# Kernel optimization log

Hardware: AMD Instinct MI355X
Metric: run time of the kernel (lower is better)

## Reference

```python
import jax, jax.numpy as jnp
import numpy as np


def _rope_tables(T, half):
    # theta_i = 10000^(-i/half), standard RoPE frequencies for head_size=2*half
    thetas = 10000.0 ** (-jnp.arange(half, dtype=jnp.float32) / half)  # (half,)
    ang = jnp.arange(T, dtype=jnp.float32)[:, None] * thetas[None, :]  # (T, half)
    return jnp.sin(ang), jnp.cos(ang)


def _apply_rope(x, sin, cos):
    # x: (B, H, T, hs); sin/cos: (T, hs//2). Interleaved pair rotation.
    xe = x[..., 0::2]
    xo = x[..., 1::2]
    s = sin[None, None, :, :]
    c = cos[None, None, :, :]
    re = xe * c - xo * s
    ro = xe * s + xo * c
    return jnp.stack([re, ro], axis=-1).reshape(x.shape)


def setup_inputs() -> dict:
    key = jax.random.key(0)
    ks = jax.random.split(key, 5)
    B, T, C, H = 4, 2048, 1024, 16
    scale = 1.0 / np.sqrt(C)
    x = jax.random.normal(ks[0], (B, T, C), dtype=jnp.float32)
    Wqkv = jax.random.normal(ks[1], (C, 3 * C), dtype=jnp.float32) * scale
    bqkv = jax.random.normal(ks[2], (3 * C,), dtype=jnp.float32) * 0.01
    Wout = jax.random.normal(ks[3], (C, C), dtype=jnp.float32) * scale
    bout = jax.random.normal(ks[4], (C,), dtype=jnp.float32) * 0.01
    return {"x": x, "Wqkv": Wqkv, "bqkv": bqkv, "Wout": Wout, "bout": bout,
            "num_heads": H}


def reference(x, Wqkv, bqkv, Wout, bout, num_heads) -> jnp.ndarray:
    B, T, C = x.shape
    H = num_heads
    hs = C // H
    norm = 1.0 / np.sqrt(hs)

    qkv = x @ Wqkv + bqkv                       # (B, T, 3C)
    qkv = qkv.reshape(B, T, 3, H, hs)
    qkv = jnp.transpose(qkv, (0, 3, 2, 1, 4))   # (B, H, 3, T, hs) = transpose(1,3)
    q, k, v = qkv[:, :, 0], qkv[:, :, 1], qkv[:, :, 2]  # each (B, H, T, hs)

    sin, cos = _rope_tables(T, hs // 2)
    q = _apply_rope(q, sin, cos)
    k = _apply_rope(k, sin, cos)

    att = jnp.einsum('bhqd,bhkd->bhqk', q, k) * norm  # (B, H, T, T)
    causal = jnp.triu(jnp.ones((T, T), dtype=bool), k=1)
    att = jnp.where(causal[None, None], -jnp.inf, att)
    att_prob = jax.nn.softmax(att, axis=-1)

    out = jnp.einsum('bhqk,bhkd->bhqd', att_prob, v)  # (B, H, T, hs)
    out = jnp.transpose(out, (0, 2, 1, 3)).reshape(B, T, C)
    return out @ Wout + bout
```

## Files before the change

kernel.cpp:

```cpp
#include <hip/hip_runtime.h>
#include <math.h>

#define B_   4
#define T_   2048
#define C_   1024
#define H_   16
#define HS   64
#define HALF 32
#define QKV_N (3 * C_)
#define M_    (B_ * T_)

using bf16x8 = __attribute__((ext_vector_type(8))) short;
using f32x4  = __attribute__((ext_vector_type(4))) float;
using f32x16 = __attribute__((ext_vector_type(16))) float;
using u16x4  = __attribute__((ext_vector_type(4))) unsigned short;
using u32x2  = __attribute__((ext_vector_type(2))) unsigned int;

__device__ __forceinline__ unsigned short f2bf(float f) {
    unsigned u = __builtin_bit_cast(unsigned, f);
    u = (u + 0x7FFFu + ((u >> 16) & 1u)) >> 16;
    return (unsigned short)u;
}
__device__ __forceinline__ float bf2f(unsigned short b) {
    return __builtin_bit_cast(float, (unsigned)b << 16);
}
__device__ __forceinline__ unsigned cvtpk_bf16(float lo, float hi_) {
    unsigned r;
    asm("v_cvt_pk_bf16_f32 %0, %1, %2" : "=v"(r) : "v"(lo), "v"(hi_));
    return r;
}
__device__ __forceinline__ void gload16(const void* g, void* l) {
    __builtin_amdgcn_global_load_lds(
        (const __attribute__((address_space(1))) unsigned int*)g,
        (__attribute__((address_space(3))) unsigned int*)l, 16, 0, 0);
}
#define WAIT_VMCNT_8() asm volatile("s_waitcnt vmcnt(8)" ::: "memory")
#define WAIT_VMCNT_4() asm volatile("s_waitcnt vmcnt(4)" ::: "memory")
#define WAIT_VMCNT_0() asm volatile("s_waitcnt vmcnt(0)" ::: "memory")

#if __has_builtin(__builtin_amdgcn_exp2f)
#define EXP2(x) __builtin_amdgcn_exp2f(x)
#else
#define EXP2(x) exp2f(x)
#endif
#define FMAX3(a, b, c) fmaxf(fmaxf((a), (b)), (c))

#define QSCALE 0.18033688011112042f

__global__ __launch_bounds__(256) void prep2_kernel(
    const float* __restrict__ x, unsigned short* __restrict__ xb,
    float2* __restrict__ tab,
    const float* __restrict__ Wqkv, const float* __restrict__ Wout,
    unsigned short* __restrict__ Wqkvt, unsigned short* __restrict__ Woutt)
{
    __shared__ float tile[32][33];
    const int bid = blockIdx.x;
    if (bid < 4096) {
        const size_t i = ((size_t)bid * 256 + threadIdx.x) * 8;
        const float4 a = *reinterpret_cast<const float4*>(&x[i]);
        const float4 b = *reinterpret_cast<const float4*>(&x[i + 4]);
        bf16x8 v;
        v[0] = f2bf(a.x); v[1] = f2bf(a.y); v[2] = f2bf(a.z); v[3] = f2bf(a.w);
        v[4] = f2bf(b.x); v[5] = f2bf(b.y); v[6] = f2bf(b.z); v[7] = f2bf(b.w);
        *reinterpret_cast<bf16x8*>(&xb[i]) = v;
        return;
    }
    if (bid < 4352) {
        const int idx = (bid - 4096) * 256 + threadIdx.x;
        const int t = idx / HALF;
        const int i = idx % HALF;
        const float theta = powf(10000.0f, -(float)i / (float)HALF);
        const float ang = (float)t * theta;
        float sn, cs;
        sincosf(ang, &sn, &cs);
        tab[idx] = make_float2(sn, cs);
        return;
    }
    const float* W;
    unsigned short* Wt;
    int N, k0, n0;
    if (bid < 7424) {
        const int r0 = bid - 4352;
        W = Wqkv; Wt = Wqkvt; N = QKV_N;
        n0 = (r0 % 96) * 32; k0 = (r0 / 96) * 32;
    } else {
        const int r0 = bid - 7424;
        W = Wout; Wt = Woutt; N = C_;
        n0 = (r0 % 32) * 32; k0 = (r0 / 32) * 32;
    }
    const int K = C_;
    const int r = threadIdx.x / 32;
    const int c = threadIdx.x % 32;
    #pragma unroll
    for (int it = 0; it < 4; ++it)
        tile[r + it * 8][c] = W[(size_t)(k0 + r + it * 8) * N + n0 + c];
    __syncthreads();
    #pragma unroll
    for (int it = 0; it < 4; ++it)
        Wt[(size_t)(n0 + r + it * 8) * K + k0 + c] = f2bf(tile[c][r + it * 8]);
}

template <int N, int K, bool BF16OUT, bool ROPE, bool VSPLIT>
__global__ __launch_bounds__(256, 4) void gemm_mfma_kernel(
    const unsigned short* __restrict__ A, const unsigned short* __restrict__ Bt,
    const float* __restrict__ bias, const float2* __restrict__ tab,
    void* __restrict__ Cout, unsigned short* __restrict__ vt, int nbx, int nby)
{
    __shared__ unsigned short As[2][128 * 32];
    __shared__ unsigned short Bs[2][128 * 32];

    const int tid  = threadIdx.x;
    const int lane = tid & 63;
    const int wave = tid >> 6;
    const int wr   = wave >> 1;
    const int wc   = wave & 1;
    const int l15  = lane & 15;
    const int l4   = lane >> 4;

    const int bid  = blockIdx.x;
    const int xcd  = bid & 7;
    const int w    = bid >> 3;
    const int cpr  = nbx >> 1;
    const int rpr  = nby >> 2;
    const int by   = ((xcd >> 1) * rpr) + (w / cpr);
    const int bx   = ((xcd & 1) * cpr) + (w % cpr);
    const int row0 = by * 128;
    const int col0 = bx * 128;

    f32x4 acc[4][4] = {};

    const int ar  = tid >> 2;
    const int sl  = tid & 3;
    const int swz = (sl ^ ((ar >> 1) & 3)) * 8;
    const unsigned short* ap = &A[(size_t)(row0 + ar) * K + swz];
    const unsigned short* bp = &Bt[(size_t)(col0 + ar) * K + swz];

    auto stage = [&](int buf, int t) {
        const unsigned short* a0 = ap + t * 32;
        const unsigned short* b0 = bp + t * 32;
        gload16(a0,          &As[buf][tid * 8]);
        gload16(a0 + 64 * K, &As[buf][(tid + 256) * 8]);
        gload16(b0,          &Bs[buf][tid * 8]);
        gload16(b0 + 64 * K, &Bs[buf][(tid + 256) * 8]);
    };

    int aoff[4], boff[4];
    #pragma unroll
    for (int mi = 0; mi < 4; ++mi) {
        const int lr = wr * 64 + mi * 16 + l15;
        aoff[mi] = lr * 32 + ((l4 ^ ((lr >> 1) & 3)) * 8);
    }
    #pragma unroll
    for (int nj = 0; nj < 4; ++nj) {
        const int lr = wc * 64 + nj * 16 + l15;
        boff[nj] = lr * 32 + ((l4 ^ ((lr >> 1) & 3)) * 8);
    }

    constexpr int nt = K / 32;
    stage(0, 0);

    for (int t = 0; t < nt; ++t) {
        const int cur = t & 1;
        if (t + 1 < nt) {
            stage(cur ^ 1, t + 1);
            WAIT_VMCNT_4();
        } else {
            WAIT_VMCNT_0();
        }
        __builtin_amdgcn_s_barrier();
        __builtin_amdgcn_sched_barrier(0);

        bf16x8 a[4], b[4];
        #pragma unroll
        for (int mi = 0; mi < 4; ++mi)
            a[mi] = *reinterpret_cast<const bf16x8*>(&As[cur][aoff[mi]]);
        #pragma unroll
        for (int nj = 0; nj < 4; ++nj)
            b[nj] = *reinterpret_cast<const bf16x8*>(&Bs[cur][boff[nj]]);
        #pragma unroll
        for (int mi = 0; mi < 4; ++mi)
            #pragma unroll
            for (int nj = 0; nj < 4; ++nj)
                acc[mi][nj] = __builtin_amdgcn_mfma_f32_16x16x32_bf16(
                    a[mi], b[nj], acc[mi][nj], 0, 0, 0);

        __builtin_amdgcn_sched_barrier(0);
        __builtin_amdgcn_s_barrier();
    }

    float bv[4];
    #pragma unroll
    for (int nj = 0; nj < 4; ++nj)
        bv[nj] = bias[col0 + wc * 64 + nj * 16 + l15];

    if (VSPLIT && col0 >= 2 * C_) {
        #pragma unroll
        for (int mi = 0; mi < 4; ++mi) {
            const int rowb = row0 + wr * 64 + mi * 16 + l4 * 4;
            const int b  = rowb >> 11;
            const int t0 = rowb & (T_ - 1);
            #pragma unroll
            for (int nj = 0; nj < 4; ++nj) {
                const int cv = col0 - 2 * C_ + wc * 64 + nj * 16 + l15;
                u16x4 pack;
                #pragma unroll
                for (int r = 0; r < 4; ++r)
                    pack[r] = f2bf(acc[mi][nj][r] + bv[nj]);
                *reinterpret_cast<u16x4*>(
                    &vt[((size_t)(b * H_ * HS + cv)) * T_ + t0]) = pack;
            }
        }
        return;
    }

    const bool doRope = ROPE && (col0 < 2 * C_);
    const bool doScaleQ = ROPE && (col0 < C_);

    #pragma unroll
    for (int mi = 0; mi < 4; ++mi) {
        #pragma unroll
        for (int r = 0; r < 4; ++r) {
            const int row = row0 + wr * 64 + mi * 16 + l4 * 4 + r;
            const int t   = row & (T_ - 1);
            #pragma unroll
            for (int nj = 0; nj < 4; ++nj) {
                const int col = col0 + wc * 64 + nj * 16 + l15;
                float v = acc[mi][nj][r] + bv[nj];
                if (doRope) {
                    const float partner = __shfl_xor(v, 1);
                    const float2 sc = tab[t * HALF + ((col & 63) >> 1)];
                    v = v * sc.y + ((col & 1) ? partner : -partner) * sc.x;
                }
                if (doScaleQ) v *= QSCALE;
                if (BF16OUT)
                    ((unsigned short*)Cout)[(size_t)row * N + col] = f2bf(v);
                else
                    ((float*)Cout)[(size_t)row * N + col] = v;
            }
        }
    }
}

__global__ __launch_bounds__(256, 2) void attn_mfma5_kernel(
    const unsigned short* __restrict__ qkv,
    const unsigned short* __restrict__ vt,
    unsigned short* __restrict__ out)
{
    __shared__ unsigned short Ks[2][128 * 64];
    __shared__ unsigned short Vs[2][64 * 128];

    const int idx = blockIdx.x;
    const int bh  = idx & 63;
    const int qp  = idx >> 6;
    const int b   = bh >> 4;
    const int h   = bh & 15;
    const int qtA = qp;
    const int qtB = 15 - qp;

    const int tid  = threadIdx.x;
    const int lane = tid & 63;
    const int w    = tid >> 6;
    const int l31  = lane & 31;
    const int hi   = lane >> 5;

    const int qwA = qtA * 128 + w * 32;
    const int qgA = qwA + l31;
    const int qwB = qtB * 128 + w * 32;
    const int qgB = qwB + l31;

    bf16x8 aqA[4], aqB[4];
    {
        const unsigned short* qpA = &qkv[(size_t)(b * T_ + qgA) * QKV_N + h * HS + hi * 8];
        const unsigned short* qpB = &qkv[(size_t)(b * T_ + qgB) * QKV_N + h * HS + hi * 8];
        #pragma unroll
        for (int kc = 0; kc < 4; ++kc) {
            aqA[kc] = *reinterpret_cast<const bf16x8*>(qpA + kc * 16);
            aqB[kc] = *reinterpret_cast<const bf16x8*>(qpB + kc * 16);
        }
    }

    f32x16 accA0 = {}, accA1 = {}, accB0 = {}, accB1 = {};
    float mA = -INFINITY, lA = 0.f, mB = -INFINITY, lB = 0.f;

    auto stageKV = [&](int buf, int it) {
        #pragma unroll
        for (int n = 0; n < 4; ++n) {
            const int r  = n * 32 + (tid >> 3);
            const int sk = ((tid & 7) ^ (r & 7)) * 8;
            gload16(&qkv[(size_t)(b * T_ + it * 128 + r) * QKV_N + C_ + h * HS + sk],
                    &Ks[buf][(n * 256 + tid) * 8]);
        }
        #pragma unroll
        for (int n = 0; n < 4; ++n) {
            const int d  = n * 16 + (tid >> 4);
            const int sv = ((tid & 15) ^ (d & 7)) * 8;
            gload16(&vt[((size_t)(bh * HS + d)) * T_ + it * 128 + sv],
                    &Vs[buf][(n * 256 + tid) * 8]);
        }
    };

    auto process = [&](const unsigned short* Kb, const unsigned short* Vb,
                       const bf16x8* aq, f32x16& a0, f32x16& a1,
                       float& mval, float& lval, int qw, int qg, int kbase) {
        f32x16 s[4] = {};
        __builtin_amdgcn_s_setprio(1);
        #pragma unroll
        for (int kc = 0; kc < 4; ++kc) {
            const int bo = kc * 32 + hi * 16;
            #pragma unroll
            for (int g = 0; g < 4; ++g) {
                const int rj = g * 32 + l31;
                const bf16x8 ak = *reinterpret_cast<const bf16x8*>(
                    &Kb[rj * 64 + ((bo ^ ((rj & 7) << 4)) >> 1)]);
                s[g] = __builtin_amdgcn_mfma_f32_32x32x16_bf16(ak, aq[kc], s[g], 0, 0, 0);
            }
        }
        __builtin_amdgcn_s_setprio(0);

        if (kbase + 127 > qw) {
            #pragma unroll
            for (int g = 0; g < 4; ++g) {
                #pragma unroll
                for (int r = 0; r < 16; ++r) {
                    const int j0 = kbase + g * 32 + (r & 3) + 8 * (r >> 2) + 4 * hi;
                    if (j0 > qg) s[g][r] = -INFINITY;
                }
            }
        }

        float tg[4];
        #pragma unroll
        for (int g = 0; g < 4; ++g) {
            const float v0 = FMAX3(s[g][0],  s[g][1],  s[g][2]);
            const float v1 = FMAX3(s[g][3],  s[g][4],  s[g][5]);
            const float v2 = FMAX3(s[g][6],  s[g][7],  s[g][8]);
            const float v3 = FMAX3(s[g][9],  s[g][10], s[g][11]);
            const float v4 = FMAX3(s[g][12], s[g][13], s[g][14]);
            tg[g] = fmaxf(FMAX3(v0, v1, v2), FMAX3(v3, v4, s[g][15]));
        }
        float tm = fmaxf(fmaxf(tg[0], tg[1]), fmaxf(tg[2], tg[3]));
        tm = fmaxf(tm, __shfl_xor(tm, 32));

        const bool upd = (tm > mval + 8.f);
        if (__ballot(upd)) {
            const float nm = upd ? tm : mval;
            const float sf = EXP2(mval - nm);
            lval *= sf;
            #pragma unroll
            for (int r = 0; r < 16; ++r) { a0[r] *= sf; a1[r] *= sf; }
            mval = nm;
        }

        float rs0 = 0.f, rs1 = 0.f, rs2 = 0.f, rs3 = 0.f;
        #pragma unroll
        for (int r = 0; r < 16; ++r) {
            s[0][r] = EXP2(s[0][r] - mval); rs0 += s[0][r];
            s[1][r] = EXP2(s[1][r] - mval); rs1 += s[1][r];
            s[2][r] = EXP2(s[2][r] - mval); rs2 += s[2][r];
            s[3][r] = EXP2(s[3][r] - mval); rs3 += s[3][r];
        }
        float rs = (rs0 + rs1) + (rs2 + rs3);
        rs += __shfl_xor(rs, 32);
        lval += rs;

        #pragma unroll
        for (int g2 = 0; g2 < 2; ++g2) {
            #pragma unroll
            for (int jt = 0; jt < 2; ++jt) {
                const int g = g2 * 2 + jt;
                #pragma unroll
                for (int c = 0; c < 2; ++c) {
                    const int e = c * 8;
                    const unsigned pa = cvtpk_bf16(s[g][e + 0], s[g][e + 1]);
                    const unsigned pb = cvtpk_bf16(s[g][e + 2], s[g][e + 3]);
                    const unsigned pc = cvtpk_bf16(s[g][e + 4], s[g][e + 5]);
                    const unsigned pd = cvtpk_bf16(s[g][e + 6], s[g][e + 7]);
                    int4 bw;
#if __has_builtin(__builtin_amdgcn_permlane32_swap)
                    const u32x2 rx = __builtin_amdgcn_permlane32_swap(pa, pc, false, false);
                    const u32x2 ry = __builtin_amdgcn_permlane32_swap(pb, pd, false, false);
                    bw.x = (int)rx[0]; bw.y = (int)ry[0];
                    bw.z = (int)rx[1]; bw.w = (int)ry[1];
#else
                    const unsigned pas = (unsigned)__shfl_xor((int)pa, 32);
                    const unsigned pbs = (unsigned)__shfl_xor((int)pb, 32);
                    const unsigned pcs = (unsigned)__shfl_xor((int)pc, 32);
                    const unsigned pds = (unsigned)__shfl_xor((int)pd, 32);
                    bw.x = (int)(hi ? pcs : pa);
                    bw.y = (int)(hi ? pds : pb);
                    bw.z = (int)(hi ? pc  : pas);
                    bw.w = (int)(hi ? pd  : pbs);
#endif
                    const bf16x8 bfrag = __builtin_bit_cast(bf16x8, bw);

                    const int lslot = g2 * 8 + (jt * 2 + c) * 2 + hi;
                    const int d0 = l31;
                    const bf16x8 av0 = *reinterpret_cast<const bf16x8*>(
                        &Vb[d0 * 128 + (lslot ^ (d0 & 7)) * 8]);
                    const int d1 = 32 + l31;
                    const bf16x8 av1 = *reinterpret_cast<const bf16x8*>(
                        &Vb[d1 * 128 + (lslot ^ (d1 & 7)) * 8]);
                    __builtin_amdgcn_s_setprio(1);
                    a0 = __builtin_amdgcn_mfma_f32_32x32x16_bf16(av0, bfrag, a0, 0, 0, 0);
                    a1 = __builtin_amdgcn_mfma_f32_32x32x16_bf16(av1, bfrag, a1, 0, 0, 0);
                    __builtin_amdgcn_s_setprio(0);
                }
            }
        }
    };

    const int nIter = qtB + 1;
    stageKV(0, 0);
    for (int it = 0; it < nIter; ++it) {
        const int cur = it & 1;
        __builtin_amdgcn_sched_barrier(0);
        if (it + 1 < nIter) {
            stageKV(cur ^ 1, it + 1);
            WAIT_VMCNT_8();
        } else {
            WAIT_VMCNT_0();
        }
        __builtin_amdgcn_s_barrier();
        __builtin_amdgcn_sched_barrier(0);

        const unsigned short* Kb = &Ks[cur][0];
        const unsigned short* Vb = &Vs[cur][0];
        const int kbase = it * 128;
        if (kbase <= qwA + 31)
            process(Kb, Vb, aqA, accA0, accA1, mA, lA, qwA, qgA, kbase);
        if (kbase <= qwB + 31)
            process(Kb, Vb, aqB, accB0, accB1, mB, lB, qwB, qgB, kbase);
        __builtin_amdgcn_sched_barrier(0);
        __builtin_amdgcn_s_barrier();
    }

    {
        const float inv = 1.0f / lA;
        unsigned short* orow = &out[(size_t)(b * T_ + qgA) * C_ + h * HS];
        #pragma unroll
        for (int g = 0; g < 4; ++g) {
            uint2 wv;
            wv.x = cvtpk_bf16(accA0[4 * g + 0] * inv, accA0[4 * g + 1] * inv);
            wv.y = cvtpk_bf16(accA0[4 * g + 2] * inv, accA0[4 * g + 3] * inv);
            *reinterpret_cast<uint2*>(&orow[8 * g + 4 * hi]) = wv;
            uint2 wv1;
            wv1.x = cvtpk_bf16(accA1[4 * g + 0] * inv, accA1[4 * g + 1] * inv);
            wv1.y = cvtpk_bf16(accA1[4 * g + 2] * inv, accA1[4 * g + 3] * inv);
            *reinterpret_cast<uint2*>(&orow[32 + 8 * g + 4 * hi]) = wv1;
        }
    }
    {
        const float inv = 1.0f / lB;
        unsigned short* orow = &out[(size_t)(b * T_ + qgB) * C_ + h * HS];
        #pragma unroll
        for (int g = 0; g < 4; ++g) {
            uint2 wv;
            wv.x = cvtpk_bf16(accB0[4 * g + 0] * inv, accB0[4 * g + 1] * inv);
            wv.y = cvtpk_bf16(accB0[4 * g + 2] * inv, accB0[4 * g + 3] * inv);
            *reinterpret_cast<uint2*>(&orow[8 * g + 4 * hi]) = wv;
            uint2 wv1;
            wv1.x = cvtpk_bf16(accB1[4 * g + 0] * inv, accB1[4 * g + 1] * inv);
            wv1.y = cvtpk_bf16(accB1[4 * g + 2] * inv, accB1[4 * g + 3] * inv);
            *reinterpret_cast<uint2*>(&orow[32 + 8 * g + 4 * hi]) = wv1;
        }
    }
}

extern "C" void kernel_launch(void* const* d_in, const int* in_sizes, int n_in,
                              void* d_out, int out_size, void* d_ws, size_t ws_size,
                              hipStream_t stream)
{
    const float* x    = (const float*)d_in[0];
    const float* Wqkv = (const float*)d_in[1];
    const float* bqkv = (const float*)d_in[2];
    const float* Wout = (const float*)d_in[3];
    const float* bout = (const float*)d_in[4];
    float* out = (float*)d_out;

    char* ws = (char*)d_ws;
    unsigned short* qkvb  = (unsigned short*)ws;
    unsigned short* xb    = (unsigned short*)(ws + 50331648);
    unsigned short* attnb = (unsigned short*)(ws + 67108864);
    unsigned short* vt_g  = (unsigned short*)(ws + 83886080);
    unsigned short* Wqkvt = (unsigned short*)(ws + 100663296);
    unsigned short* Woutt = (unsigned short*)(ws + 106954752);
    float2* tab           = (float2*)(ws + 109051904);

    prep2_kernel<<<8448, 256, 0, stream>>>(x, xb, tab, Wqkv, Wout, Wqkvt, Woutt);

    gemm_mfma_kernel<QKV_N, C_, true, true, true>
        <<<(M_ / 128) * (QKV_N / 128), 256, 0, stream>>>(
        xb, Wqkvt, bqkv, tab, qkvb, vt_g, QKV_N / 128, M_ / 128);

    attn_mfma5_kernel<<<B_ * H_ * (T_ / 256), 256, 0, stream>>>(qkvb, vt_g, attnb);

    gemm_mfma_kernel<C_, C_, false, false, false>
        <<<(M_ / 128) * (C_ / 128), 256, 0, stream>>>(
        attnb, Woutt, bout, nullptr, out, nullptr, C_ / 128, M_ / 128);
}
```

Before: 167.2 us.

## Replace GEMMs with 256x256-tile, 8-wave, four-phase ping-pong MFMA kernel

Both projection GEMMs move from 128x128 tiles with 4 waves to 256x256 tiles with 8 waves and a BK of 64. The K loop is split into four phases, each issuing one quarter-tile global-to-LDS prefetch and then running one 128x64 quadrant of MFMAs, with s_setprio raising priority around the MFMA bursts. The aim is more operand reuse per LDS byte and better overlap of loads with compute. The cost is 128 KB of LDS per block, one block per CU, and far fewer blocks: the output projection launches only 128 blocks and the QKV projection 384, which risks underfilling the GPU or leaving a tail wave.

```diff
diff --git a/kernel.cpp b/kernel.cpp
--- a/kernel.cpp
+++ b/kernel.cpp
@@ -37,6 +37,7 @@
 #define WAIT_VMCNT_8() asm volatile("s_waitcnt vmcnt(8)" ::: "memory")
 #define WAIT_VMCNT_4() asm volatile("s_waitcnt vmcnt(4)" ::: "memory")
 #define WAIT_VMCNT_0() asm volatile("s_waitcnt vmcnt(0)" ::: "memory")
+#define WAIT_LGKM_0()  asm volatile("s_waitcnt lgkmcnt(0)" ::: "memory")
 
 #if __has_builtin(__builtin_amdgcn_exp2f)
 #define EXP2(x) __builtin_amdgcn_exp2f(x)
@@ -101,19 +102,21 @@
 }
 
 template <int N, int K, bool BF16OUT, bool ROPE, bool VSPLIT>
-__global__ __launch_bounds__(256, 4) void gemm_mfma_kernel(
+__global__ __launch_bounds__(512, 1) void gemm_8ph_kernel(
     const unsigned short* __restrict__ A, const unsigned short* __restrict__ Bt,
     const float* __restrict__ bias, const float2* __restrict__ tab,
     void* __restrict__ Cout, unsigned short* __restrict__ vt, int nbx, int nby)
 {
-    __shared__ unsigned short As[2][128 * 32];
-    __shared__ unsigned short Bs[2][128 * 32];
+    __shared__ unsigned short As0[2][128 * 64];
+    __shared__ unsigned short As1[2][128 * 64];
+    __shared__ unsigned short Bs0[2][128 * 64];
+    __shared__ unsigned short Bs1[2][128 * 64];
 
     const int tid  = threadIdx.x;
     const int lane = tid & 63;
     const int wave = tid >> 6;
-    const int wr   = wave >> 1;
-    const int wc   = wave & 1;
+    const int wr   = wave >> 2;
+    const int wc   = wave & 3;
     const int l15  = lane & 15;
     const int l4   = lane >> 4;
 
@@ -124,88 +127,176 @@
     const int rpr  = nby >> 2;
     const int by   = ((xcd >> 1) * rpr) + (w / cpr);
     const int bx   = ((xcd & 1) * cpr) + (w % cpr);
-    const int row0 = by * 128;
-    const int col0 = bx * 128;
-
-    f32x4 acc[4][4] = {};
-
-    const int ar  = tid >> 2;
-    const int sl  = tid & 3;
-    const int swz = (sl ^ ((ar >> 1) & 3)) * 8;
-    const unsigned short* ap = &A[(size_t)(row0 + ar) * K + swz];
-    const unsigned short* bp = &Bt[(size_t)(col0 + ar) * K + swz];
-
-    auto stage = [&](int buf, int t) {
-        const unsigned short* a0 = ap + t * 32;
-        const unsigned short* b0 = bp + t * 32;
-        gload16(a0,          &As[buf][tid * 8]);
-        gload16(a0 + 64 * K, &As[buf][(tid + 256) * 8]);
-        gload16(b0,          &Bs[buf][tid * 8]);
-        gload16(b0 + 64 * K, &Bs[buf][(tid + 256) * 8]);
+    const int row0 = by * 256;
+    const int col0 = bx * 256;
+
+    const int lr0 = tid >> 3,          sl0 = tid & 7;
+    const int lr1 = (tid + 512) >> 3,  sl1 = (tid + 512) & 7;
+    const int kc0 = (sl0 ^ (lr0 & 7)) * 8;
+    const int kc1 = (sl1 ^ (lr1 & 7)) * 8;
+    const int dA0 = tid * 8;
+    const int dA1 = (tid + 512) * 8;
+    const unsigned short* apS0 = &A[(size_t)(row0 + (lr0 >> 6) * 128 + (lr0 & 63)) * K + kc0];
+    const unsigned short* apS1 = &A[(size_t)(row0 + (lr1 >> 6) * 128 + (lr1 & 63)) * K + kc1];
+    const unsigned short* bpS0 = &Bt[(size_t)(col0 + (lr0 >> 5) * 64 + (lr0 & 31)) * K + kc0];
+    const unsigned short* bpS1 = &Bt[(size_t)(col0 + (lr1 >> 5) * 64 + (lr1 & 31)) * K + kc1];
+
+    auto stA0 = [&](int buf, int t) {
+        gload16(apS0 + t * 64,            &As0[buf][dA0]);
+        gload16(apS1 + t * 64,            &As0[buf][dA1]);
     };
-
-    int aoff[4], boff[4];
+    auto stA1 = [&](int buf, int t) {
+        gload16(apS0 + t * 64 + 64 * K,   &As1[buf][dA0]);
+        gload16(apS1 + t * 64 + 64 * K,   &As1[buf][dA1]);
+    };
+    auto stB0 = [&](int buf, int t) {
+        gload16(bpS0 + t * 64,            &Bs0[buf][dA0]);
+        gload16(bpS1 + t * 64,            &Bs0[buf][dA1]);
+    };
+    auto stB1 = [&](int buf, int t) {
+        gload16(bpS0 + t * 64 + 32 * K,   &Bs1[buf][dA0]);
+        gload16(bpS1 + t * 64 + 32 * K,   &Bs1[buf][dA1]);
+    };
+
+    int aoff[2][4], boff[2][2];
     #pragma unroll
-    for (int mi = 0; mi < 4; ++mi) {
-        const int lr = wr * 64 + mi * 16 + l15;
-        aoff[mi] = lr * 32 + ((l4 ^ ((lr >> 1) & 3)) * 8);
-    }
-    #pragma unroll
-    for (int nj = 0; nj < 4; ++nj) {
-        const int lr = wc * 64 + nj * 16 + l15;
-        boff[nj] = lr * 32 + ((l4 ^ ((lr >> 1) & 3)) * 8);
-    }
-
-    constexpr int nt = K / 32;
-    stage(0, 0);
+    for (int kk = 0; kk < 2; ++kk) {
+        #pragma unroll
+        for (int mi = 0; mi < 4; ++mi) {
+            const int lr = wr * 64 + mi * 16 + l15;
+            aoff[kk][mi] = lr * 64 + (((kk * 4 + l4) ^ (lr & 7)) * 8);
+        }
+        #pragma unroll
+        for (int nj = 0; nj < 2; ++nj) {
+            const int lr = wc * 32 + nj * 16 + l15;
+            boff[kk][nj] = lr * 64 + (((kk * 4 + l4) ^ (lr & 7)) * 8);
+        }
+    }
+
+    f32x4 acc[8][4] = {};
+    constexpr int nt = K / 64;
+
+    stA0(0, 0); stB0(0, 0); stB1(0, 0); stA1(0, 0);
+    WAIT_VMCNT_4();
+    __builtin_amdgcn_s_barrier();
+
+    bf16x8 a[2][4], b01[2][2], b23[2][2];
 
     for (int t = 0; t < nt; ++t) {
         const int cur = t & 1;
-        if (t + 1 < nt) {
-            stage(cur ^ 1, t + 1);
-            WAIT_VMCNT_4();
-        } else {
-            WAIT_VMCNT_0();
-        }
-        __builtin_amdgcn_s_barrier();
-        __builtin_amdgcn_sched_barrier(0);
-
-        bf16x8 a[4], b[4];
-        #pragma unroll
-        for (int mi = 0; mi < 4; ++mi)
-            a[mi] = *reinterpret_cast<const bf16x8*>(&As[cur][aoff[mi]]);
-        #pragma unroll
-        for (int nj = 0; nj < 4; ++nj)
-            b[nj] = *reinterpret_cast<const bf16x8*>(&Bs[cur][boff[nj]]);
-        #pragma unroll
-        for (int mi = 0; mi < 4; ++mi)
-            #pragma unroll
-            for (int nj = 0; nj < 4; ++nj)
-                acc[mi][nj] = __builtin_amdgcn_mfma_f32_16x16x32_bf16(
-                    a[mi], b[nj], acc[mi][nj], 0, 0, 0);
-
-        __builtin_amdgcn_sched_barrier(0);
-        __builtin_amdgcn_s_barrier();
-    }
+        const int nxt = cur ^ 1;
+        const int tn  = (t + 1 < nt) ? t + 1 : 0;
+
+        #pragma unroll
+        for (int kk = 0; kk < 2; ++kk) {
+            #pragma unroll
+            for (int mi = 0; mi < 4; ++mi)
+                a[kk][mi] = *reinterpret_cast<const bf16x8*>(&As0[cur][aoff[kk][mi]]);
+            #pragma unroll
+            for (int nj = 0; nj < 2; ++nj)
+                b01[kk][nj] = *reinterpret_cast<const bf16x8*>(&Bs0[cur][boff[kk][nj]]);
+        }
+        stA0(nxt, tn);
+        WAIT_VMCNT_4();
+        __builtin_amdgcn_s_barrier();
+        WAIT_LGKM_0();
+        __builtin_amdgcn_sched_barrier(0);
+        __builtin_amdgcn_s_setprio(1);
+        #pragma unroll
+        for (int kk = 0; kk < 2; ++kk)
+            #pragma unroll
+            for (int mi = 0; mi < 4; ++mi)
+                #pragma unroll
+                for (int nj = 0; nj < 2; ++nj)
+                    acc[mi][nj] = __builtin_amdgcn_mfma_f32_16x16x32_bf16(
+                        a[kk][mi], b01[kk][nj], acc[mi][nj], 0, 0, 0);
+        __builtin_amdgcn_s_setprio(0);
+        __builtin_amdgcn_sched_barrier(0);
+        __builtin_amdgcn_s_barrier();
+
+        #pragma unroll
+        for (int kk = 0; kk < 2; ++kk)
+            #pragma unroll
+            for (int nj = 0; nj < 2; ++nj)
+                b23[kk][nj] = *reinterpret_cast<const bf16x8*>(&Bs1[cur][boff[kk][nj]]);
+        stB0(nxt, tn);
+        WAIT_VMCNT_4();
+        __builtin_amdgcn_s_barrier();
+        WAIT_LGKM_0();
+        __builtin_amdgcn_sched_barrier(0);
+        __builtin_amdgcn_s_setprio(1);
+        #pragma unroll
+        for (int kk = 0; kk < 2; ++kk)
+            #pragma unroll
+            for (int mi = 0; mi < 4; ++mi)
+                #pragma unroll
+                for (int nj = 0; nj < 2; ++nj)
+                    acc[mi][2 + nj] = __builtin_amdgcn_mfma_f32_16x16x32_bf16(
+                        a[kk][mi], b23[kk][nj], acc[mi][2 + nj], 0, 0, 0);
+        __builtin_amdgcn_s_setprio(0);
+        __builtin_amdgcn_sched_barrier(0);
+        __builtin_amdgcn_s_barrier();
+
+        #pragma unroll
+        for (int kk = 0; kk < 2; ++kk)
+            #pragma unroll
+            for (int mi = 0; mi < 4; ++mi)
+                a[kk][mi] = *reinterpret_cast<const bf16x8*>(&As1[cur][aoff[kk][mi]]);
+        stB1(nxt, tn);
+        WAIT_VMCNT_4();
+        __builtin_amdgcn_s_barrier();
+        WAIT_LGKM_0();
+        __builtin_amdgcn_sched_barrier(0);
+        __builtin_amdgcn_s_setprio(1);
+        #pragma unroll
+        for (int kk = 0; kk < 2; ++kk)
+            #pragma unroll
+            for (int mi = 0; mi < 4; ++mi)
+                #pragma unroll
+                for (int nj = 0; nj < 2; ++nj)
+                    acc[4 + mi][nj] = __builtin_amdgcn_mfma_f32_16x16x32_bf16(
+                        a[kk][mi], b01[kk][nj], acc[4 + mi][nj], 0, 0, 0);
+        __builtin_amdgcn_s_setprio(0);
+        __builtin_amdgcn_sched_barrier(0);
+        __builtin_amdgcn_s_barrier();
+
+        stA1(nxt, tn);
+        WAIT_VMCNT_4();
+        __builtin_amdgcn_s_barrier();
+        __builtin_amdgcn_sched_barrier(0);
+        __builtin_amdgcn_s_setprio(1);
+        #pragma unroll
+        for (int kk = 0; kk < 2; ++kk)
+            #pragma unroll
+            for (int mi = 0; mi < 4; ++mi)
+                #pragma unroll
+                for (int nj = 0; nj < 2; ++nj)
+                    acc[4 + mi][2 + nj] = __builtin_amdgcn_mfma_f32_16x16x32_bf16(
+                        a[kk][mi], b23[kk][nj], acc[4 + mi][2 + nj], 0, 0, 0);
+        __builtin_amdgcn_s_setprio(0);
+        __builtin_amdgcn_sched_barrier(0);
+        __builtin_amdgcn_s_barrier();
+    }
+    WAIT_VMCNT_0();
 
     float bv[4];
     #pragma unroll
-    for (int nj = 0; nj < 4; ++nj)
-        bv[nj] = bias[col0 + wc * 64 + nj * 16 + l15];
+    for (int nf = 0; nf < 4; ++nf)
+        bv[nf] = bias[col0 + wc * 64 + nf * 16 + l15];
 
     if (VSPLIT && col0 >= 2 * C_) {
         #pragma unroll
-        for (int mi = 0; mi < 4; ++mi) {
-            const int rowb = row0 + wr * 64 + mi * 16 + l4 * 4;
+        for (int mf = 0; mf < 8; ++mf) {
+            const int rowb = row0 + wr * 128 + mf * 16 + l4 * 4;
             const int b  = rowb >> 11;
             const int t0 = rowb & (T_ - 1);
             #pragma unroll
-            for (int nj = 0; nj < 4; ++nj) {
-                const int cv = col0 - 2 * C_ + wc * 64 + nj * 16 + l15;
+            for (int nf = 0; nf < 4; ++nf) {
+                const int cv = col0 - 2 * C_ + wc * 64 + nf * 16 + l15;
                 u16x4 pack;
                 #pragma unroll
                 for (int r = 0; r < 4; ++r)
-                    pack[r] = f2bf(acc[mi][nj][r] + bv[nj]);
+                    pack[r] = f2bf(acc[mf][nf][r] + bv[nf]);
                 *reinterpret_cast<u16x4*>(
                     &vt[((size_t)(b * H_ * HS + cv)) * T_ + t0]) = pack;
             }
@@ -217,15 +308,15 @@
     const bool doScaleQ = ROPE && (col0 < C_);
 
     #pragma unroll
-    for (int mi = 0; mi < 4; ++mi) {
+    for (int mf = 0; mf < 8; ++mf) {
         #pragma unroll
         for (int r = 0; r < 4; ++r) {
-            const int row = row0 + wr * 64 + mi * 16 + l4 * 4 + r;
+            const int row = row0 + wr * 128 + mf * 16 + l4 * 4 + r;
             const int t   = row & (T_ - 1);
             #pragma unroll
-            for (int nj = 0; nj < 4; ++nj) {
-                const int col = col0 + wc * 64 + nj * 16 + l15;
-                float v = acc[mi][nj][r] + bv[nj];
+            for (int nf = 0; nf < 4; ++nf) {
+                const int col = col0 + wc * 64 + nf * 16 + l15;
+                float v = acc[mf][nf][r] + bv[nf];
                 if (doRope) {
                     const float partner = __shfl_xor(v, 1);
                     const float2 sc = tab[t * HALF + ((col & 63) >> 1)];
@@ -488,13 +579,13 @@
 
     prep2_kernel<<<8448, 256, 0, stream>>>(x, xb, tab, Wqkv, Wout, Wqkvt, Woutt);
 
-    gemm_mfma_kernel<QKV_N, C_, true, true, true>
-        <<<(M_ / 128) * (QKV_N / 128), 256, 0, stream>>>(
-        xb, Wqkvt, bqkv, tab, qkvb, vt_g, QKV_N / 128, M_ / 128);
+    gemm_8ph_kernel<QKV_N, C_, true, true, true>
+        <<<(M_ / 256) * (QKV_N / 256), 512, 0, stream>>>(
+        xb, Wqkvt, bqkv, tab, qkvb, vt_g, QKV_N / 256, M_ / 256);
 
     attn_mfma5_kernel<<<B_ * H_ * (T_ / 256), 256, 0, stream>>>(qkvb, vt_g, attnb);
 
-    gemm_mfma_kernel<C_, C_, false, false, false>
-        <<<(M_ / 128) * (C_ / 128), 256, 0, stream>>>(
-        attnb, Woutt, bout, nullptr, out, nullptr, C_ / 128, M_ / 128);
-}
+    gemm_8ph_kernel<C_, C_, false, false, false>
+        <<<(M_ / 256) * (C_ / 256), 512, 0, stream>>>(
+        attnb, Woutt, bout, nullptr, out, nullptr, C_ / 256, M_ / 256);
+}
```

Result: slower. 172.4 us (+3.1%).

## Fuse fp32-to-bf16 conversion of x into the QKV GEMM A-tile load

Applied to the files above, without the earlier changes.

Removes the separate x conversion pass from the prep kernel and has the QKV GEMM read fp32 activations directly, converting to bf16 in registers before writing swizzled LDS tiles. This avoids writing and rereading a bf16 copy of x. In exchange, the GEMM loads twice as many bytes per A tile through registers instead of direct-to-LDS loads, adding register pressure and extra wait points in the pipeline. The output projection GEMM is split into its own simplified template.

```diff
diff --git a/kernel.cpp b/kernel.cpp
--- a/kernel.cpp
+++ b/kernel.cpp
@@ -35,8 +35,11 @@
         (__attribute__((address_space(3))) unsigned int*)l, 16, 0, 0);
 }
 #define WAIT_VMCNT_8() asm volatile("s_waitcnt vmcnt(8)" ::: "memory")
+#define WAIT_VMCNT_6() asm volatile("s_waitcnt vmcnt(6)" ::: "memory")
 #define WAIT_VMCNT_4() asm volatile("s_waitcnt vmcnt(4)" ::: "memory")
+#define WAIT_VMCNT_2() asm volatile("s_waitcnt vmcnt(2)" ::: "memory")
 #define WAIT_VMCNT_0() asm volatile("s_waitcnt vmcnt(0)" ::: "memory")
+#define WAIT_LGKM_0()  asm volatile("s_waitcnt lgkmcnt(0)" ::: "memory")
 
 #if __has_builtin(__builtin_amdgcn_exp2f)
 #define EXP2(x) __builtin_amdgcn_exp2f(x)
@@ -47,26 +50,15 @@
 
 #define QSCALE 0.18033688011112042f
 
-__global__ __launch_bounds__(256) void prep2_kernel(
-    const float* __restrict__ x, unsigned short* __restrict__ xb,
+__global__ __launch_bounds__(256) void prep3_kernel(
     float2* __restrict__ tab,
     const float* __restrict__ Wqkv, const float* __restrict__ Wout,
     unsigned short* __restrict__ Wqkvt, unsigned short* __restrict__ Woutt)
 {
     __shared__ float tile[32][33];
     const int bid = blockIdx.x;
-    if (bid < 4096) {
-        const size_t i = ((size_t)bid * 256 + threadIdx.x) * 8;
-        const float4 a = *reinterpret_cast<const float4*>(&x[i]);
-        const float4 b = *reinterpret_cast<const float4*>(&x[i + 4]);
-        bf16x8 v;
-        v[0] = f2bf(a.x); v[1] = f2bf(a.y); v[2] = f2bf(a.z); v[3] = f2bf(a.w);
-        v[4] = f2bf(b.x); v[5] = f2bf(b.y); v[6] = f2bf(b.z); v[7] = f2bf(b.w);
-        *reinterpret_cast<bf16x8*>(&xb[i]) = v;
-        return;
-    }
-    if (bid < 4352) {
-        const int idx = (bid - 4096) * 256 + threadIdx.x;
+    if (bid < 256) {
+        const int idx = bid * 256 + threadIdx.x;
         const int t = idx / HALF;
         const int i = idx % HALF;
         const float theta = powf(10000.0f, -(float)i / (float)HALF);
@@ -79,12 +71,12 @@
     const float* W;
     unsigned short* Wt;
     int N, k0, n0;
-    if (bid < 7424) {
-        const int r0 = bid - 4352;
+    if (bid < 3328) {
+        const int r0 = bid - 256;
         W = Wqkv; Wt = Wqkvt; N = QKV_N;
         n0 = (r0 % 96) * 32; k0 = (r0 / 96) * 32;
     } else {
-        const int r0 = bid - 7424;
+        const int r0 = bid - 3328;
         W = Wout; Wt = Woutt; N = C_;
         n0 = (r0 % 32) * 32; k0 = (r0 / 32) * 32;
     }
@@ -100,11 +92,12 @@
         Wt[(size_t)(n0 + r + it * 8) * K + k0 + c] = f2bf(tile[c][r + it * 8]);
 }
 
-template <int N, int K, bool BF16OUT, bool ROPE, bool VSPLIT>
-__global__ __launch_bounds__(256, 4) void gemm_mfma_kernel(
-    const unsigned short* __restrict__ A, const unsigned short* __restrict__ Bt,
+template <int N, int K>
+__global__ __launch_bounds__(256, 4) void gemm_qkv_kernel(
+    const float* __restrict__ A, const unsigned short* __restrict__ Bt,
     const float* __restrict__ bias, const float2* __restrict__ tab,
-    void* __restrict__ Cout, unsigned short* __restrict__ vt, int nbx, int nby)
+    unsigned short* __restrict__ Cout, unsigned short* __restrict__ vt,
+    int nbx, int nby)
 {
     __shared__ unsigned short As[2][128 * 32];
     __shared__ unsigned short Bs[2][128 * 32];
@@ -129,17 +122,40 @@
 
     f32x4 acc[4][4] = {};
 
-    const int ar  = tid >> 2;
-    const int sl  = tid & 3;
-    const int swz = (sl ^ ((ar >> 1) & 3)) * 8;
-    const unsigned short* ap = &A[(size_t)(row0 + ar) * K + swz];
-    const unsigned short* bp = &Bt[(size_t)(col0 + ar) * K + swz];
-
-    auto stage = [&](int buf, int t) {
-        const unsigned short* a0 = ap + t * 32;
+    const int ar = tid >> 1;
+    const int ah = tid & 1;
+    const float* apg = &A[(size_t)(row0 + ar) * K + ah * 16];
+    const int asw = (ar >> 1) & 3;
+    const int awo0 = ar * 32 + (((ah * 2 + 0) ^ asw) * 8);
+    const int awo1 = ar * 32 + (((ah * 2 + 1) ^ asw) * 8);
+    float4 ar4[4];
+
+    const int br  = tid >> 2;
+    const int bsl = tid & 3;
+    const int bswz = (bsl ^ ((br >> 1) & 3)) * 8;
+    const unsigned short* bp = &Bt[(size_t)(col0 + br) * K + bswz];
+
+    auto loadA = [&](int t) {
+        const float* p = apg + t * 32;
+        #pragma unroll
+        for (int u = 0; u < 4; ++u)
+            ar4[u] = *reinterpret_cast<const float4*>(p + u * 4);
+    };
+    auto writeA = [&](int buf) {
+        int4 w0, w1;
+        w0.x = (int)cvtpk_bf16(ar4[0].x, ar4[0].y);
+        w0.y = (int)cvtpk_bf16(ar4[0].z, ar4[0].w);
+        w0.z = (int)cvtpk_bf16(ar4[1].x, ar4[1].y);
+        w0.w = (int)cvtpk_bf16(ar4[1].z, ar4[1].w);
+        w1.x = (int)cvtpk_bf16(ar4[2].x, ar4[2].y);
+        w1.y = (int)cvtpk_bf16(ar4[2].z, ar4[2].w);
+        w1.z = (int)cvtpk_bf16(ar4[3].x, ar4[3].y);
+        w1.w = (int)cvtpk_bf16(ar4[3].z, ar4[3].w);
+        *reinterpret_cast<int4*>(&As[buf][awo0]) = w0;
+        *reinterpret_cast<int4*>(&As[buf][awo1]) = w1;
+    };
+    auto stageB = [&](int buf, int t) {
         const unsigned short* b0 = bp + t * 32;
-        gload16(a0,          &As[buf][tid * 8]);
-        gload16(a0 + 64 * K, &As[buf][(tid + 256) * 8]);
         gload16(b0,          &Bs[buf][tid * 8]);
         gload16(b0 + 64 * K, &Bs[buf][(tid + 256) * 8]);
     };
@@ -157,13 +173,20 @@
     }
 
     constexpr int nt = K / 32;
-    stage(0, 0);
+
+    loadA(0);
+    stageB(0, 0);
+    WAIT_VMCNT_2();
+    writeA(0);
+    WAIT_LGKM_0();
+    __builtin_amdgcn_s_barrier();
 
     for (int t = 0; t < nt; ++t) {
         const int cur = t & 1;
         if (t + 1 < nt) {
-            stage(cur ^ 1, t + 1);
-            WAIT_VMCNT_4();
+            loadA(t + 1);
+            stageB(cur ^ 1, t + 1);
+            WAIT_VMCNT_6();
         } else {
             WAIT_VMCNT_0();
         }
@@ -184,6 +207,11 @@
                 acc[mi][nj] = __builtin_amdgcn_mfma_f32_16x16x32_bf16(
                     a[mi], b[nj], acc[mi][nj], 0, 0, 0);
 
+        if (t + 1 < nt) {
+            WAIT_VMCNT_2();
+            writeA(cur ^ 1);
+        }
+        WAIT_LGKM_0();
         __builtin_amdgcn_sched_barrier(0);
         __builtin_amdgcn_s_barrier();
     }
@@ -193,7 +221,7 @@
     for (int nj = 0; nj < 4; ++nj)
         bv[nj] = bias[col0 + wc * 64 + nj * 16 + l15];
 
-    if (VSPLIT && col0 >= 2 * C_) {
+    if (col0 >= 2 * C_) {
         #pragma unroll
         for (int mi = 0; mi < 4; ++mi) {
             const int rowb = row0 + wr * 64 + mi * 16 + l4 * 4;
@@ -213,8 +241,7 @@
         return;
     }
 
-    const bool doRope = ROPE && (col0 < 2 * C_);
-    const bool doScaleQ = ROPE && (col0 < C_);
+    const bool doScaleQ = (col0 < C_);
 
     #pragma unroll
     for (int mi = 0; mi < 4; ++mi) {
@@ -226,12 +253,119 @@
             for (int nj = 0; nj < 4; ++nj) {
                 const int col = col0 + wc * 64 + nj * 16 + l15;
                 float v = acc[mi][nj][r] + bv[nj];
-                if (doRope) {
+                {
                     const float partner = __shfl_xor(v, 1);
                     const float2 sc = tab[t * HALF + ((col & 63) >> 1)];
                     v = v * sc.y + ((col & 1) ? partner : -partner) * sc.x;
                 }
                 if (doScaleQ) v *= QSCALE;
+                Cout[(size_t)row * N + col] = f2bf(v);
+            }
+        }
+    }
+}
+
+template <int N, int K, bool BF16OUT>
+__global__ __launch_bounds__(256, 4) void gemm_2ph_kernel(
+    const unsigned short* __restrict__ A, const unsigned short* __restrict__ Bt,
+    const float* __restrict__ bias, void* __restrict__ Cout, int nbx, int nby)
+{
+    __shared__ unsigned short As[2][128 * 32];
+    __shared__ unsigned short Bs[2][128 * 32];
+
+    const int tid  = threadIdx.x;
+    const int lane = tid & 63;
+    const int wave = tid >> 6;
+    const int wr   = wave >> 1;
+    const int wc   = wave & 1;
+    const int l15  = lane & 15;
+    const int l4   = lane >> 4;
+
+    const int bid  = blockIdx.x;
+    const int xcd  = bid & 7;
+    const int w    = bid >> 3;
+    const int cpr  = nbx >> 1;
+    const int rpr  = nby >> 2;
+    const int by   = ((xcd >> 1) * rpr) + (w / cpr);
+    const int bx   = ((xcd & 1) * cpr) + (w % cpr);
+    const int row0 = by * 128;
+    const int col0 = bx * 128;
+
+    f32x4 acc[4][4] = {};
+
+    const int ar  = tid >> 2;
+    const int sl  = tid & 3;
+    const int swz = (sl ^ ((ar >> 1) & 3)) * 8;
+    const unsigned short* ap = &A[(size_t)(row0 + ar) * K + swz];
+    const unsigned short* bp = &Bt[(size_t)(col0 + ar) * K + swz];
+
+    auto stage = [&](int buf, int t) {
+        const unsigned short* a0 = ap + t * 32;
+        const unsigned short* b0 = bp + t * 32;
+        gload16(a0,          &As[buf][tid * 8]);
+        gload16(a0 + 64 * K, &As[buf][(tid + 256) * 8]);
+        gload16(b0,          &Bs[buf][tid * 8]);
+        gload16(b0 + 64 * K, &Bs[buf][(tid + 256) * 8]);
+    };
+
+    int aoff[4], boff[4];
+    #pragma unroll
+    for (int mi = 0; mi < 4; ++mi) {
+        const int lr = wr * 64 + mi * 16 + l15;
+        aoff[mi] = lr * 32 + ((l4 ^ ((lr >> 1) & 3)) * 8);
+    }
+    #pragma unroll
+    for (int nj = 0; nj < 4; ++nj) {
+        const int lr = wc * 64 + nj * 16 + l15;
+        boff[nj] = lr * 32 + ((l4 ^ ((lr >> 1) & 3)) * 8);
+    }
+
+    constexpr int nt = K / 32;
+    stage(0, 0);
+
+    for (int t = 0; t < nt; ++t) {
+        const int cur = t & 1;
+        if (t + 1 < nt) {
+            stage(cur ^ 1, t + 1);
+            WAIT_VMCNT_4();
+        } else {
+            WAIT_VMCNT_0();
+        }
+        __builtin_amdgcn_s_barrier();
+        __builtin_amdgcn_sched_barrier(0);
+
+        bf16x8 a[4], b[4];
+        #pragma unroll
+        for (int mi = 0; mi < 4; ++mi)
+            a[mi] = *reinterpret_cast<const bf16x8*>(&As[cur][aoff[mi]]);
+        #pragma unroll
+        for (int nj = 0; nj < 4; ++nj)
+            b[nj] = *reinterpret_cast<const bf16x8*>(&Bs[cur][boff[nj]]);
+        #pragma unroll
+        for (int mi = 0; mi < 4; ++mi)
+            #pragma unroll
+            for (int nj = 0; nj < 4; ++nj)
+                acc[mi][nj] = __builtin_amdgcn_mfma_f32_16x16x32_bf16(
+                    a[mi], b[nj], acc[mi][nj], 0, 0, 0);
+
+        __builtin_amdgcn_sched_barrier(0);
+        __builtin_amdgcn_s_barrier();
+    }
+
+    float bv[4];
+    #pragma unroll
+    for (int nj = 0; nj < 4; ++nj)
+        bv[nj] = bias[col0 + wc * 64 + nj * 16 + l15];
+
+    #pragma unroll
+    for (int mi = 0; mi < 4; ++mi) {
+        #pragma unroll
+        for (int r = 0; r < 4; ++r) {
+            const int row = row0 + wr * 64 + mi * 16 + l4 * 4 + r;
+            #pragma unroll
+            for (int nj = 0; nj < 4; ++nj) {
+                const int col = col0 + wc * 64 + nj * 16 + l15;
+                const float v = acc[mi][nj][r] + bv[nj];
                 if (BF16OUT)
                     ((unsigned short*)Cout)[(size_t)row * N + col] = f2bf(v);
                 else
@@ -479,22 +613,21 @@
 
     char* ws = (char*)d_ws;
     unsigned short* qkvb  = (unsigned short*)ws;
-    unsigned short* xb    = (unsigned short*)(ws + 50331648);
     unsigned short* attnb = (unsigned short*)(ws + 67108864);
     unsigned short* vt_g  = (unsigned short*)(ws + 83886080);
     unsigned short* Wqkvt = (unsigned short*)(ws + 100663296);
     unsigned short* Woutt = (unsigned short*)(ws + 106954752);
     float2* tab           = (float2*)(ws + 109051904);
 
-    prep2_kernel<<<8448, 256, 0, stream>>>(x, xb, tab, Wqkv, Wout, Wqkvt, Woutt);
-
-    gemm_mfma_kernel<QKV_N, C_, true, true, true>
+    prep3_kernel<<<4352, 256, 0, stream>>>(tab, Wqkv, Wout, Wqkvt, Woutt);
+
+    gemm_qkv_kernel<QKV_N, C_>
         <<<(M_ / 128) * (QKV_N / 128), 256, 0, stream>>>(
-        xb, Wqkvt, bqkv, tab, qkvb, vt_g, QKV_N / 128, M_ / 128);
+        x, Wqkvt, bqkv, tab, qkvb, vt_g, QKV_N / 128, M_ / 128);
 
     attn_mfma5_kernel<<<B_ * H_ * (T_ / 256), 256, 0, stream>>>(qkvb, vt_g, attnb);
 
-    gemm_mfma_kernel<C_, C_, false, false, false>
+    gemm_2ph_kernel<C_, C_, false>
         <<<(M_ / 128) * (C_ / 128), 256, 0, stream>>>(
-        attnb, Woutt, bout, nullptr, out, nullptr, C_ / 128, M_ / 128);
-}
+        attnb, Woutt, bout, out, C_ / 128, M_ / 128);
+}
```

After: 178.0 us. +6.5%, slower.
